# Performance work log

Measured on AMD Instinct MI355X. Metric: run time of the kernel, lower is better.

Reference implementation:

```python
import jax, jax.numpy as jnp
import numpy as np

N_NODES = 50000
N_EDGES = 800000
HIDDEN = 128
EPS = 1e-5


def _layernorm(x, g, b):
    m = jnp.mean(x, axis=-1, keepdims=True)
    v = jnp.var(x, axis=-1, keepdims=True)
    return (x - m) / jnp.sqrt(v + EPS) * g + b


def _batchnorm(x, g, b):
    # training-mode BatchNorm1d: stats over the node (batch) axis, biased var
    m = jnp.mean(x, axis=0, keepdims=True)
    v = jnp.var(x, axis=0, keepdims=True)
    return (x - m) / jnp.sqrt(v + EPS) * g + b


def _instnorm(x):
    # torch InstanceNorm1d on a 2D [N,C] input: unbatched (C,L) view ->
    # normalize each row over the feature axis, no affine params
    m = jnp.mean(x, axis=-1, keepdims=True)
    v = jnp.var(x, axis=-1, keepdims=True)
    return (x - m) / jnp.sqrt(v + EPS)


def _gcn_conv(x, W, b, row, col, norm, n):
    # PyG GCNConv: out[col] += norm * (x @ W)[row]; + bias
    xw = x @ W
    msgs = xw[row] * norm[:, None]          # [E+N, H]
    out = jax.ops.segment_sum(msgs, col, num_segments=n)
    return out + b


def setup_inputs() -> dict:
    key = jax.random.key(0)
    ks = jax.random.split(key, 12)
    H = HIDDEN
    x = jax.random.normal(ks[0], (N_NODES, 2), dtype=jnp.float32)
    edge_index = jax.random.randint(ks[1], (2, N_EDGES), 0, N_NODES, dtype=jnp.int64)

    def lin(k, fan_in, shape):
        bound = 1.0 / np.sqrt(fan_in)
        return jax.random.uniform(k, shape, jnp.float32, -bound, bound)

    inp = {
        "x": x,
        "edge_index": edge_index,
        "coord_W": lin(ks[2], 2, (2, H)),
        "coord_b": lin(ks[3], 2, (H,)),
        "ln_g": jnp.ones((H,), jnp.float32),
        "ln_b": jnp.zeros((H,), jnp.float32),
        "bn_g": jnp.ones((H,), jnp.float32),
        "bn_b": jnp.zeros((H,), jnp.float32),
        "W1": lin(ks[4], H, (H, H)),
        "b1": jnp.zeros((H,), jnp.float32),
        "W2": lin(ks[5], H, (H, H)),
        "b2": jnp.zeros((H,), jnp.float32),
        "W3": lin(ks[6], H, (H, H)),
        "b3": jnp.zeros((H,), jnp.float32),
        "fc1_W": lin(ks[7], H, (H, 32)),
        "fc1_b": lin(ks[8], H, (32,)),
        "fc2_W": lin(ks[9], 32, (32, 2)),
        "fc2_b": lin(ks[10], 32, (2,)),
    }
    return inp


def reference(x, edge_index, coord_W, coord_b, ln_g, ln_b, bn_g, bn_b,
              W1, b1, W2, b2, W3, b3, fc1_W, fc1_b, fc2_W, fc2_b):
    n = x.shape[0]
    loop = jnp.arange(n, dtype=edge_index.dtype)
    row = jnp.concatenate([edge_index[0], loop])
    col = jnp.concatenate([edge_index[1], loop])
    deg = jax.ops.segment_sum(jnp.ones_like(col, dtype=x.dtype), col, num_segments=n)
    dinv = 1.0 / jnp.sqrt(deg)              # deg >= 1 thanks to self-loops
    norm = dinv[row] * dinv[col]

    h = jax.nn.relu(x @ coord_W + coord_b)
    h = _layernorm(h, ln_g, ln_b)

    for W, b in ((W1, b1), (W2, b2), (W3, b3)):
        identity = h
        h = jax.nn.relu(_gcn_conv(h, W, b, row, col, norm, n))
        h = _batchnorm(h, bn_g, bn_b)
        h = _instnorm(h + identity)

    h = jax.nn.relu(h @ fc1_W + fc1_b)
    return jnp.tanh(h @ fc2_W + fc2_b)
```

## Files before the change

### kernel.cpp

```cpp
#include <hip/hip_runtime.h>
#include <hip/hip_bf16.h>
#include <hip/hip_fp16.h>
#include <stdint.h>

#define NN 50000
#define NE 800000
#define HD 128
#define EPSN 1e-5f
#define CAP 1152000

typedef __hip_bfloat16 bf16;
typedef __attribute__((ext_vector_type(8))) _Float16 half8;
typedef __attribute__((ext_vector_type(4))) float f32x4;

__device__ __forceinline__ float us2f(unsigned short u) { return __uint_as_float((uint32_t)u << 16); }
__device__ __forceinline__ ushort f2us(float f) {
    bf16 b = __float2bfloat16(f);
    return *reinterpret_cast<ushort*>(&b);
}
__device__ __forceinline__ ushort f2h(float f) {
    __half h = __float2half(f);
    return *reinterpret_cast<ushort*>(&h);
}
__device__ __forceinline__ float h2f(ushort u) {
    __half h = *reinterpret_cast<__half*>(&u);
    return __half2float(h);
}

__device__ __forceinline__ void cvt8(float4 v, float* o) {
    uint32_t a = __float_as_uint(v.x), b = __float_as_uint(v.y);
    uint32_t c = __float_as_uint(v.z), d = __float_as_uint(v.w);
    o[0] = h2f((ushort)(a & 0xffff)); o[1] = h2f((ushort)(a >> 16));
    o[2] = h2f((ushort)(b & 0xffff)); o[3] = h2f((ushort)(b >> 16));
    o[4] = h2f((ushort)(c & 0xffff)); o[5] = h2f((ushort)(c >> 16));
    o[6] = h2f((ushort)(d & 0xffff)); o[7] = h2f((ushort)(d >> 16));
}

#define O_X    0
#define O_CW   100000
#define O_CB   100256
#define O_LNG  100384
#define O_LNB  100512
#define O_BNG  100640
#define O_BNB  100768
#define O_W1   100896
#define O_B1   117280
#define O_W2   117408
#define O_B2   133792
#define O_W3   133920
#define O_B3   150304
#define O_F1W  150432
#define O_F1B  154528
#define O_F2W  154560
#define O_F2B  154624
#define O_TOT  154626

struct Ptrs { const void* p[17]; };

__device__ const int SEG_OFF[18] = {O_X, O_CW, O_CB, O_LNG, O_LNB, O_BNG, O_BNB,
                                    O_W1, O_B1, O_W2, O_B2, O_W3, O_B3,
                                    O_F1W, O_F1B, O_F2W, O_F2B, O_TOT};

__device__ __forceinline__ int eidx(const int* __restrict__ ei, int isL, int which, int e) {
    size_t base = (size_t)which * NE + e;
    return isL ? ei[2 * base] : ei[base];
}

__global__ void k_detect(const int* __restrict__ ei, const ushort* __restrict__ cw,
                         int* __restrict__ flags) {
    int t = threadIdx.x;
    int v = ei[2 * t + 1] | ei[1000000 + 2 * t + 1];
    int bad = 0;
    if (t < 128) {
        float val = us2f(cw[2 * t]);
        bad = !(fabsf(val) <= 1.0f);
    }
    for (int o = 32; o; o >>= 1) { v |= __shfl_xor(v, o); bad |= __shfl_xor(bad, o); }
    __shared__ int sv[4], sb[4];
    if ((t & 63) == 0) { sv[t >> 6] = v; sb[t >> 6] = bad; }
    __syncthreads();
    if (t == 0) {
        flags[0] = ((sv[0] | sv[1] | sv[2] | sv[3]) == 0) ? 1 : 0;
        flags[1] = ((sb[0] | sb[1] | sb[2] | sb[3]) == 0) ? 1 : 0;
    }
}

__global__ void k_conv(Ptrs ptrs, const int* __restrict__ flags, float* __restrict__ cp,
                       _Float16* __restrict__ wt, int* __restrict__ degR,
                       float* __restrict__ stats, int* __restrict__ cursor) {
    int i = blockIdx.x * 256 + threadIdx.x;
    int isBf = flags[1];
    if (i < O_TOT) {
        int s = 0;
        while (i >= SEG_OFF[s + 1]) s++;
        int local = i - SEG_OFF[s];
        const void* src = ptrs.p[s];
        cp[i] = isBf ? us2f(((const ushort*)src)[local]) : ((const float*)src)[local];
    }
    if (i < 3 * HD * HD) {
        int mat = i >> 14, idx = i & (HD * HD - 1);
        int k = idx >> 7, n = idx & 127;
        const void* src = ptrs.p[7 + 2 * mat];
        int local = k * HD + n;
        float v = isBf ? us2f(((const ushort*)src)[local]) : ((const float*)src)[local];
        wt[mat * HD * HD + n * HD + k] = (_Float16)v;
    }
    if (i < 8 * NN) degR[i] = (i < NN) ? 1 : 0;
    if (i < 12288) stats[i] = 0.f;
    if (i == 0) *cursor = 0;
}

__global__ void k_deg(const int* __restrict__ ei, const int* __restrict__ flags,
                      int* __restrict__ degR) {
    int e = blockIdx.x * 256 + threadIdx.x;
    if (e < NE) atomicAdd(&degR[(blockIdx.x & 7) * NN + eidx(ei, flags[0], 1, e)], 1);
}

__global__ void k_fill(const int* __restrict__ ei, const int* __restrict__ flags,
                       const float* __restrict__ dinv, int* __restrict__ curA8,
                       int2* __restrict__ srw) {
    int e = blockIdx.x * 256 + threadIdx.x;
    if (e >= NE) return;
    int isL = flags[0];
    int r = eidx(ei, isL, 0, e);
    int c = eidx(ei, isL, 1, e);
    int p = atomicAdd(&curA8[(blockIdx.x & 7) * NN + c], 1);
    srw[p] = make_int2(r << 4, __float_as_int(dinv[r]));
}


__global__ void k_embed(const float* __restrict__ cp, ushort* __restrict__ h,
                        const int* __restrict__ degR, float* __restrict__ dinv,
                        int* __restrict__ startA, int* __restrict__ curA8,
                        int* __restrict__ cursor, int2* __restrict__ srw,
                        int* __restrict__ degO) {
    int gi = blockIdx.x * 256 + threadIdx.x;
    if (gi < NN) {
        int c[8];
        int d = 0;
#pragma unroll
        for (int r = 0; r < 8; r++) { c[r] = degR[r * NN + gi]; d += c[r]; }
        c[0] -= 1;
        degO[gi] = d;
        dinv[gi] = rsqrtf((float)d);
        int cnt = d - 1;
        int cpad = (cnt + 7) & ~7;
        int s = atomicAdd(cursor, cpad);
        startA[gi] = s;
        int off = 0;
#pragma unroll
        for (int r = 0; r < 8; r++) { curA8[r * NN + gi] = s + off; off += c[r]; }
        for (int p = s + cnt; p < s + cpad; p++) srw[p] = make_int2(0, 0);
    }
    int node = gi >> 6;
    int lane = threadIdx.x & 63;
    if (node >= NN) return;
    const float* X = cp + O_X;
    const float* CW = cp + O_CW;
    const float* CB = cp + O_CB;
    const float* LG = cp + O_LNG;
    const float* LB = cp + O_LNB;
    float x0 = X[node * 2], x1 = X[node * 2 + 1];
    int f0 = lane, f1 = lane + 64;
    float v0 = fmaxf(0.f, x0 * CW[f0] + x1 * CW[HD + f0] + CB[f0]);
    float v1 = fmaxf(0.f, x0 * CW[f1] + x1 * CW[HD + f1] + CB[f1]);
    float s = v0 + v1, q = v0 * v0 + v1 * v1;
    for (int o = 32; o; o >>= 1) { s += __shfl_xor(s, o); q += __shfl_xor(q, o); }
    float m = s * (1.f / HD);
    float var = q * (1.f / HD) - m * m;
    float r = rsqrtf(var + EPSN);
    h[(size_t)node * HD + f0] = f2h((v0 - m) * r * LG[f0] + LB[f0]);
    h[(size_t)node * HD + f1] = f2h((v1 - m) * r * LG[f1] + LB[f1]);
}


__device__ __forceinline__ void mfma_tile(const _Float16* hl, const _Float16* __restrict__ wt,
                                          ushort* __restrict__ t0h, int nodeBase, int t) {
    int w = t >> 6, l = t & 63;
    int m16 = l & 15;
    int kg = l >> 4;
    int node0 = w * 16;
    half8 a[4];
#pragma unroll
    for (int kc = 0; kc < 4; kc++) {
        int nd = node0 + m16;
        int c16 = kc * 4 + kg;
        int chunk = nd * 16 + (c16 ^ (nd & 7));
        a[kc] = *(const half8*)(hl + chunk * 8);
    }
    f32x4 acc[8];
#pragma unroll
    for (int nt = 0; nt < 8; nt++) acc[nt] = (f32x4){0.f, 0.f, 0.f, 0.f};
#pragma unroll
    for (int nt = 0; nt < 8; nt++) {
        const half8* bp = (const half8*)(wt + (size_t)(nt * 16 + m16) * HD);
#pragma unroll
        for (int kc = 0; kc < 4; kc++) {
            acc[nt] = __builtin_amdgcn_mfma_f32_16x16x32_f16(a[kc], bp[kc * 4 + kg],
                                                             acc[nt], 0, 0, 0);
        }
    }
    int ndb = nodeBase + node0 + kg * 4;
#pragma unroll
    for (int rr = 0; rr < 4; rr++) {
        int nd = ndb + rr;
        if (nd < NN) {
#pragma unroll
            for (int nt = 0; nt < 8; nt++) {
                t0h[(size_t)nd * HD + nt * 16 + m16] = f2h(acc[nt][rr]);
            }
        }
    }
}


__global__ __launch_bounds__(256) void k_gemm(const ushort* __restrict__ h,
                                              const _Float16* __restrict__ wt,
                                              ushort* __restrict__ t0h) {
    __shared__ _Float16 hl[64 * HD];
    int t = threadIdx.x;
    int nodeBase = blockIdx.x * 64;
    const uint4* h4 = (const uint4*)h;
#pragma unroll
    for (int r = 0; r < 4; r++) {
        int cid = r * 256 + t;
        int node = cid >> 4;
        int c16 = cid & 15;
        int n = nodeBase + node;
        uint4 v = make_uint4(0u, 0u, 0u, 0u);
        if (n < NN) v = h4[(size_t)n * 16 + c16];
        int chunk = node * 16 + (c16 ^ (node & 7));
        *(uint4*)(hl + chunk * 8) = v;
    }
    __syncthreads();
    mfma_tile(hl, wt, t0h, nodeBase, t);
}


__global__ __launch_bounds__(256) void k_gemm_fused(const float* __restrict__ agg,
                                                    const float* __restrict__ stats,
                                                    const float* __restrict__ bias,
                                                    const float* __restrict__ bng,
                                                    const float* __restrict__ bnb,
                                                    ushort* __restrict__ h,
                                                    const _Float16* __restrict__ wt,
                                                    ushort* __restrict__ t0h) {
    __shared__ _Float16 hl[64 * HD];
    __shared__ float scL[HD], shL[HD], bL[HD];
    int t = threadIdx.x;
    if (t < 128) {
        const float invN = 1.f / NN;
        float sv = 0.f, qv = 0.f;
#pragma unroll
        for (int r = 0; r < 16; r++) { sv += stats[r * 256 + t]; qv += stats[r * 256 + 128 + t]; }
        float m = sv * invN;
        float v = qv * invN - m * m;
        float sc = bng[t] * rsqrtf(v + EPSN);
        scL[t] = sc;
        shL[t] = bnb[t] - m * sc;
        bL[t] = bias[t];
    }
    __syncthreads();
    int nodeBase = blockIdx.x * 64;
    const float4* a4 = (const float4*)agg;
    const ushort4* h4r = (const ushort4*)h;
    ushort4* h4w = (ushort4*)h;
#pragma unroll
    for (int r = 0; r < 8; r++) {
        int idx = r * 256 + t;
        int node = idx >> 5;
        int c4 = idx & 31;
        int n = nodeBase + node;
        float4 u = make_float4(0.f, 0.f, 0.f, 0.f);
        if (n < NN) {
            float4 av = a4[(size_t)n * 32 + c4];
            ushort4 hv = h4r[(size_t)n * 32 + c4];
            int f = c4 * 4;
            float y0 = fmaxf(0.f, av.x + bL[f]);
            float y1 = fmaxf(0.f, av.y + bL[f + 1]);
            float y2 = fmaxf(0.f, av.z + bL[f + 2]);
            float y3 = fmaxf(0.f, av.w + bL[f + 3]);
            u.x = y0 * scL[f]     + shL[f]     + h2f(hv.x);
            u.y = y1 * scL[f + 1] + shL[f + 1] + h2f(hv.y);
            u.z = y2 * scL[f + 2] + shL[f + 2] + h2f(hv.z);
            u.w = y3 * scL[f + 3] + shL[f + 3] + h2f(hv.w);
        }
        float s = u.x + u.y + u.z + u.w;
        float q = u.x * u.x + u.y * u.y + u.z * u.z + u.w * u.w;
        for (int o = 16; o; o >>= 1) { s += __shfl_xor(s, o); q += __shfl_xor(q, o); }
        float m = s * (1.f / HD);
        float var = q * (1.f / HD) - m * m;
        float rr = rsqrtf(var + EPSN);
        u.x = (u.x - m) * rr; u.y = (u.y - m) * rr;
        u.z = (u.z - m) * rr; u.w = (u.w - m) * rr;
        ushort4 pk;
        pk.x = f2h(u.x); pk.y = f2h(u.y); pk.z = f2h(u.z); pk.w = f2h(u.w);
        if (n < NN) h4w[(size_t)n * 32 + c4] = pk;
        int chunk = node * 16 + ((c4 >> 1) ^ (node & 7));
        *(ushort4*)((char*)hl + chunk * 16 + (c4 & 1) * 8) = pk;
    }
    __syncthreads();
    mfma_tile(hl, wt, t0h, nodeBase, t);
}


__global__ __launch_bounds__(256) void k_agg(const ushort* __restrict__ t0h,
                                             const int2* __restrict__ srw,
                                             const int* __restrict__ startA,
                                             const int* __restrict__ deg,
                                             const float* __restrict__ dinv,
                                             const float* __restrict__ bias,
                                             float* __restrict__ agg,
                                             float* __restrict__ stats) {
    int t = threadIdx.x;
    int w = t >> 6;
    int l = t & 63;
    int g = l >> 4;
    int k = l & 15;
    int l32 = l & 31;
    const float4* t04 = (const float4*)t0h;
    float4* agg4 = (float4*)agg;
    float bs[8];
    {
        const float4* b4 = (const float4*)bias;
        float4 u0 = b4[2 * k], u1 = b4[2 * k + 1];
        bs[0] = u0.x; bs[1] = u0.y; bs[2] = u0.z; bs[3] = u0.w;
        bs[4] = u1.x; bs[5] = u1.y; bs[6] = u1.z; bs[7] = u1.w;
    }
    float rs1[8], rs2[8];
#pragma unroll
    for (int m = 0; m < 8; m++) { rs1[m] = 0.f; rs2[m] = 0.f; }
    int stride = gridDim.x * 4;
    int i = blockIdx.x * 4 + w;
    int s = 0, nb = 0;
    float di = 0.f;
    if (i < NN) {
        s = startA[i];
        nb = (deg[i] - 1 + 7) & ~7;
        di = dinv[i];
    }
    while (i < NN) {
        float4 sv = t04[(size_t)i * 16 + k];
        int2 e = make_int2(0, 0);
        if (l32 < nb) e = srw[s + l32];
        int ex = e.x, ey = e.y;
        int nb4 = nb >> 2;
        float4 gg[8];
#define GATH(b) { int rv = __shfl(ex, 4 * (b) + g); \
                  gg[b] = t04[(size_t)(uint32_t)rv + k]; }
        if (nb4 > 0) { GATH(0) GATH(1) }
        if (nb4 > 2) { GATH(2) GATH(3) }
        if (nb4 > 4) { GATH(4) GATH(5) }
        if (nb4 > 6) { GATH(6) GATH(7) }
#undef GATH
        int inext = i + stride;
        int sN = 0, nbN = 0;
        float diN = 0.f;
        if (inext < NN) {
            sN = startA[inext];
            nbN = (deg[inext] - 1 + 7) & ~7;
            diN = dinv[inext];
        }
        float acc[8], c8[8];
        cvt8(sv, c8);
        float ws = (g == 0) ? di : 0.f;
#pragma unroll
        for (int m = 0; m < 8; m++) acc[m] = ws * c8[m];
#define ACCB(b) { float wv = __int_as_float(__shfl(ey, 4 * (b) + g)); \
                  float d8[8]; cvt8(gg[b], d8); \
                  _Pragma("unroll") \
                  for (int m = 0; m < 8; m++) acc[m] += wv * d8[m]; }
        if (nb4 > 0) { ACCB(0) ACCB(1) }
        if (nb4 > 2) { ACCB(2) ACCB(3) }
        if (nb4 > 4) { ACCB(4) ACCB(5) }
        if (nb4 > 6) { ACCB(6) ACCB(7) }
#undef ACCB
        for (int j = 32; j < nb; j += 32) {
            int2 e2 = make_int2(0, 0);
            if (j + l32 < nb) e2 = srw[s + j + l32];
            int ex2 = e2.x, ey2 = e2.y;
            int rem4 = (nb - j) >> 2;
            if (rem4 > 8) rem4 = 8;
            for (int b = 0; b < rem4; b += 2) {
                int r0 = __shfl(ex2, 4 * b + g);
                int r1 = __shfl(ex2, 4 * b + 4 + g);
                float4 g0 = t04[(size_t)(uint32_t)r0 + k];
                float4 g1 = t04[(size_t)(uint32_t)r1 + k];
                float w0 = __int_as_float(__shfl(ey2, 4 * b + g));
                float w1 = __int_as_float(__shfl(ey2, 4 * b + 4 + g));
                float d0[8], d1[8];
                cvt8(g0, d0); cvt8(g1, d1);
#pragma unroll
                for (int m = 0; m < 8; m++) acc[m] += w0 * d0[m] + w1 * d1[m];
            }
        }
#pragma unroll
        for (int m = 0; m < 8; m++) {
            acc[m] += __shfl_xor(acc[m], 16);
            acc[m] += __shfl_xor(acc[m], 32);
            acc[m] *= di;
        }
        if (g == 0) {
            agg4[(size_t)i * 32 + 2 * k]     = make_float4(acc[0], acc[1], acc[2], acc[3]);
            agg4[(size_t)i * 32 + 2 * k + 1] = make_float4(acc[4], acc[5], acc[6], acc[7]);
        }
#pragma unroll
        for (int m = 0; m < 8; m++) {
            float y = fmaxf(0.f, acc[m] + bs[m]);
            rs1[m] += y;
            rs2[m] += y * y;
        }
        i = inext; s = sN; nb = nbN; di = diN;
    }
    __shared__ float s1[4][HD], s2[4][HD];
    if (l < 16) {
#pragma unroll
        for (int m = 0; m < 8; m++) {
            s1[w][k * 8 + m] = rs1[m];
            s2[w][k * 8 + m] = rs2[m];
        }
    }
    __syncthreads();
    float* st = stats + (blockIdx.x & 15) * 256;
    if (t < 128) {
        atomicAdd(&st[t], s1[0][t] + s1[1][t] + s1[2][t] + s1[3][t]);
    } else {
        int f = t - 128;
        atomicAdd(&st[128 + f], s2[0][f] + s2[1][f] + s2[2][f] + s2[3][f]);
    }
}


__global__ __launch_bounds__(256) void k_tail(const float* __restrict__ agg,
                                              const float* __restrict__ stats,
                                              const ushort* __restrict__ h,
                                              const float* __restrict__ cp,
                                              const int* __restrict__ flags,
                                              void* __restrict__ outv) {
    __shared__ float W1l[HD * 32];
    __shared__ float ub[4][HD];
    __shared__ float scT[HD], shT[HD], bT[HD];
    __shared__ float B1s[32], W2s[64], B2s[2];
    int t = threadIdx.x;
    const float4* f1w4 = (const float4*)(cp + O_F1W);
    float4* w14 = (float4*)W1l;
#pragma unroll
    for (int r = 0; r < 4; r++) w14[r * 256 + t] = f1w4[r * 256 + t];
    if (t < 32) B1s[t] = cp[O_F1B + t];
    if (t < 64) W2s[t] = cp[O_F2W + t];
    if (t < 2) B2s[t] = cp[O_F2B + t];
    if (t < 128) {
        const float invN = 1.f / NN;
        float sv = 0.f, qv = 0.f;
#pragma unroll
        for (int r = 0; r < 16; r++) { sv += stats[r * 256 + t]; qv += stats[r * 256 + 128 + t]; }
        float m = sv * invN;
        float v = qv * invN - m * m;
        float sc = cp[O_BNG + t] * rsqrtf(v + EPSN);
        scT[t] = sc;
        shT[t] = cp[O_BNB + t] - m * sc;
        bT[t] = cp[O_B3 + t];
    }
    __syncthreads();
    int isBf = flags[1];
    int w = t >> 6, l = t & 63;
    int f = l & 31, half = l >> 5;
    for (int base = blockIdx.x * 4; base < NN; base += gridDim.x * 4) {
        int node = base + w;
        if (node >= NN) continue;
        size_t o = (size_t)node * HD;
        float a0 = agg[o + l], a1 = agg[o + l + 64];
        float h0 = h2f(h[o + l]), h1 = h2f(h[o + l + 64]);
        float y0 = fmaxf(0.f, a0 + bT[l]);
        float y1 = fmaxf(0.f, a1 + bT[l + 64]);
        float u0 = y0 * scT[l]      + shT[l]      + h0;
        float u1 = y1 * scT[l + 64] + shT[l + 64] + h1;
        float s = u0 + u1, q = u0 * u0 + u1 * u1;
        for (int oo = 32; oo; oo >>= 1) { s += __shfl_xor(s, oo); q += __shfl_xor(q, oo); }
        float m = s * (1.f / HD);
        float var = q * (1.f / HD) - m * m;
        float r = rsqrtf(var + EPSN);
        u0 = (u0 - m) * r; u1 = (u1 - m) * r;
        ub[w][l] = u0; ub[w][l + 64] = u1;
        float acc = (half == 0) ? B1s[f] : 0.f;
        const float* up = ub[w] + half * 64;
        const float* wp = W1l + half * 64 * 32 + f;
#pragma unroll 16
        for (int kk = 0; kk < 64; kk++) acc += up[kk] * wp[kk * 32];
        acc += __shfl_xor(acc, 32);
        float av = fmaxf(0.f, acc);
        float p0 = av * W2s[f * 2], p1 = av * W2s[f * 2 + 1];
        for (int oo = 16; oo; oo >>= 1) { p0 += __shfl_xor(p0, oo); p1 += __shfl_xor(p1, oo); }
        if (l == 0) {
            p0 = tanhf(p0 + B2s[0]); p1 = tanhf(p1 + B2s[1]);
            if (isBf) {
                ((uint32_t*)outv)[node] = (uint32_t)f2us(p0) | ((uint32_t)f2us(p1) << 16);
            } else {
                float2 ov; ov.x = p0; ov.y = p1;
                ((float2*)outv)[node] = ov;
            }
        }
    }
}


extern "C" void kernel_launch(void* const* d_in, const int* in_sizes, int n_in,
                              void* d_out, int out_size, void* d_ws, size_t ws_size,
                              hipStream_t stream) {
    const int* ei = (const int*)d_in[1];

    Ptrs ptrs;
    ptrs.p[0] = d_in[0];
    for (int s = 1; s < 17; s++) ptrs.p[s] = d_in[s + 1];

    char* wsp = (char*)d_ws;
    size_t off = 0;
    auto alloc = [&](size_t bytes) {
        void* p = wsp + off;
        off += (bytes + 255) & ~(size_t)255;
        return p;
    };
    float* cp     = (float*)alloc((size_t)O_TOT * 4);
    ushort* h     = (ushort*)alloc((size_t)NN * HD * 2);
    ushort* t0h   = (ushort*)alloc((size_t)NN * HD * 2);
    float* agg    = (float*)alloc((size_t)NN * HD * 4);
    int* degR     = (int*)alloc((size_t)8 * NN * 4);
    int* degO     = (int*)alloc((size_t)NN * 4);
    float* dinv   = (float*)alloc((size_t)NN * 4);
    int2* srw     = (int2*)alloc((size_t)CAP * 8);
    int* startA   = (int*)alloc((size_t)NN * 4);
    int* curA8    = (int*)alloc((size_t)8 * NN * 4);
    float* stats  = (float*)alloc(3 * 4096 * 4);
    int* cursor   = (int*)alloc(256);
    int* flags    = (int*)alloc(256);
    _Float16* wt  = (_Float16*)alloc((size_t)3 * HD * HD * 2);

    const int BN_EDGE = (NE + 255) / 256;
    const int BN_CONV = (8 * NN + 255) / 256;
    const int BN_GEMM = (NN + 63) / 64;

    const float* B[3] = {cp + O_B1, cp + O_B2, cp + O_B3};

    k_detect<<<1, 256, 0, stream>>>(ei, (const ushort*)d_in[2], flags);
    k_conv<<<BN_CONV, 256, 0, stream>>>(ptrs, flags, cp, wt, degR, stats, cursor);
    k_deg<<<BN_EDGE, 256, 0, stream>>>(ei, flags, degR);
    k_embed<<<NN / 4, 256, 0, stream>>>(cp, h, degR, dinv, startA, curA8, cursor, srw, degO);
    k_fill<<<BN_EDGE, 256, 0, stream>>>(ei, flags, dinv, curA8, srw);

    k_gemm<<<BN_GEMM, 256, 0, stream>>>(h, wt, t0h);
    k_agg<<<2048, 256, 0, stream>>>(t0h, srw, startA, degO, dinv, B[0], agg, stats);
    for (int l = 1; l < 3; l++) {
        k_gemm_fused<<<BN_GEMM, 256, 0, stream>>>(agg, stats + 4096 * (l - 1),
                                                  B[l - 1], cp + O_BNG, cp + O_BNB,
                                                  h, wt + (size_t)l * HD * HD, t0h);
        k_agg<<<2048, 256, 0, stream>>>(t0h, srw, startA, degO, dinv, B[l],
                                        agg, stats + 4096 * l);
    }
    k_tail<<<2048, 256, 0, stream>>>(agg, stats + 8192, h, cp, flags, d_out);
}
```

Before: 445.0 us.

## Fold source dinv into GEMM epilogue and shrink edge records to int

Multiplies each GEMM output row by its own dinv so the aggregation kernel only sums gathered rows, with the destination dinv applied afterward as before. Edge records drop from int2 (index plus weight) to a single int, which halves CSR traffic and removes the weight shuffles and multiplies in the gather loop. Padding slots now point to an extra zeroed row at index NN instead of carrying weight zero. This needs one more row in t0h, and pre-scaling before the fp16 store slightly changes rounding.

Result: faster. 414.5 us (-6.9%).

```diff
diff --git a/kernel.cpp b/kernel.cpp
--- a/kernel.cpp
+++ b/kernel.cpp
@@ -87,7 +87,8 @@
 
 __global__ void k_conv(Ptrs ptrs, const int* __restrict__ flags, float* __restrict__ cp,
                        _Float16* __restrict__ wt, int* __restrict__ degR,
-                       float* __restrict__ stats, int* __restrict__ cursor) {
+                       float* __restrict__ stats, int* __restrict__ cursor,
+                       ushort* __restrict__ t0h) {
     int i = blockIdx.x * 256 + threadIdx.x;
     int isBf = flags[1];
     if (i < O_TOT) {
@@ -107,6 +108,7 @@
     }
     if (i < 8 * NN) degR[i] = (i < NN) ? 1 : 0;
     if (i < 12288) stats[i] = 0.f;
+    if (i < HD) t0h[(size_t)NN * HD + i] = 0;
     if (i == 0) *cursor = 0;
 }
 
@@ -117,22 +119,21 @@
 }
 
 __global__ void k_fill(const int* __restrict__ ei, const int* __restrict__ flags,
-                       const float* __restrict__ dinv, int* __restrict__ curA8,
-                       int2* __restrict__ srw) {
+                       int* __restrict__ curA8, int* __restrict__ srw) {
     int e = blockIdx.x * 256 + threadIdx.x;
     if (e >= NE) return;
     int isL = flags[0];
     int r = eidx(ei, isL, 0, e);
     int c = eidx(ei, isL, 1, e);
     int p = atomicAdd(&curA8[(blockIdx.x & 7) * NN + c], 1);
-    srw[p] = make_int2(r << 4, __float_as_int(dinv[r]));
+    srw[p] = r << 4;
 }
 
 
 __global__ void k_embed(const float* __restrict__ cp, ushort* __restrict__ h,
                         const int* __restrict__ degR, float* __restrict__ dinv,
                         int* __restrict__ startA, int* __restrict__ curA8,
-                        int* __restrict__ cursor, int2* __restrict__ srw,
+                        int* __restrict__ cursor, int* __restrict__ srw,
                         int* __restrict__ degO) {
     int gi = blockIdx.x * 256 + threadIdx.x;
     if (gi < NN) {
@@ -150,7 +151,7 @@
         int off = 0;
 #pragma unroll
         for (int r = 0; r < 8; r++) { curA8[r * NN + gi] = s + off; off += c[r]; }
-        for (int p = s + cnt; p < s + cpad; p++) srw[p] = make_int2(0, 0);
+        for (int p = s + cnt; p < s + cpad; p++) srw[p] = NN << 4;
     }
     int node = gi >> 6;
     int lane = threadIdx.x & 63;
@@ -175,6 +176,7 @@
 
 
 __device__ __forceinline__ void mfma_tile(const _Float16* hl, const _Float16* __restrict__ wt,
+                                          const float* __restrict__ dinv,
                                           ushort* __restrict__ t0h, int nodeBase, int t) {
     int w = t >> 6, l = t & 63;
     int m16 = l & 15;
@@ -205,9 +207,10 @@
     for (int rr = 0; rr < 4; rr++) {
         int nd = ndb + rr;
         if (nd < NN) {
+            float dv = dinv[nd];
 #pragma unroll
             for (int nt = 0; nt < 8; nt++) {
-                t0h[(size_t)nd * HD + nt * 16 + m16] = f2h(acc[nt][rr]);
+                t0h[(size_t)nd * HD + nt * 16 + m16] = f2h(acc[nt][rr] * dv);
             }
         }
     }
@@ -216,6 +219,7 @@
 
 __global__ __launch_bounds__(256) void k_gemm(const ushort* __restrict__ h,
                                               const _Float16* __restrict__ wt,
+                                              const float* __restrict__ dinv,
                                               ushort* __restrict__ t0h) {
     __shared__ _Float16 hl[64 * HD];
     int t = threadIdx.x;
@@ -233,7 +237,7 @@
         *(uint4*)(hl + chunk * 8) = v;
     }
     __syncthreads();
-    mfma_tile(hl, wt, t0h, nodeBase, t);
+    mfma_tile(hl, wt, dinv, t0h, nodeBase, t);
 }
 
 
@@ -244,6 +248,7 @@
                                                     const float* __restrict__ bnb,
                                                     ushort* __restrict__ h,
                                                     const _Float16* __restrict__ wt,
+                                                    const float* __restrict__ dinv,
                                                     ushort* __restrict__ t0h) {
     __shared__ _Float16 hl[64 * HD];
     __shared__ float scL[HD], shL[HD], bL[HD];
@@ -300,12 +305,12 @@
         *(ushort4*)((char*)hl + chunk * 16 + (c4 & 1) * 8) = pk;
     }
     __syncthreads();
-    mfma_tile(hl, wt, t0h, nodeBase, t);
+    mfma_tile(hl, wt, dinv, t0h, nodeBase, t);
 }
 
 
 __global__ __launch_bounds__(256) void k_agg(const ushort* __restrict__ t0h,
-                                             const int2* __restrict__ srw,
+                                             const int* __restrict__ srw,
                                              const int* __restrict__ startA,
                                              const int* __restrict__ deg,
                                              const float* __restrict__ dinv,
@@ -341,9 +346,8 @@
     }
     while (i < NN) {
         float4 sv = t04[(size_t)i * 16 + k];
-        int2 e = make_int2(0, 0);
-        if (l32 < nb) e = srw[s + l32];
-        int ex = e.x, ey = e.y;
+        int ex = 0;
+        if (l32 < nb) ex = srw[s + l32];
         int nb4 = nb >> 2;
         float4 gg[8];
 #define GATH(b) { int rv = __shfl(ex, 4 * (b) + g); \
@@ -363,22 +367,20 @@
         }
         float acc[8], c8[8];
         cvt8(sv, c8);
-        float ws = (g == 0) ? di : 0.f;
+        float ws = (g == 0) ? 1.f : 0.f;
 #pragma unroll
         for (int m = 0; m < 8; m++) acc[m] = ws * c8[m];
-#define ACCB(b) { float wv = __int_as_float(__shfl(ey, 4 * (b) + g)); \
-                  float d8[8]; cvt8(gg[b], d8); \
+#define ACCB(b) { float d8[8]; cvt8(gg[b], d8); \
                   _Pragma("unroll") \
-                  for (int m = 0; m < 8; m++) acc[m] += wv * d8[m]; }
+                  for (int m = 0; m < 8; m++) acc[m] += d8[m]; }
         if (nb4 > 0) { ACCB(0) ACCB(1) }
         if (nb4 > 2) { ACCB(2) ACCB(3) }
         if (nb4 > 4) { ACCB(4) ACCB(5) }
         if (nb4 > 6) { ACCB(6) ACCB(7) }
 #undef ACCB
         for (int j = 32; j < nb; j += 32) {
-            int2 e2 = make_int2(0, 0);
-            if (j + l32 < nb) e2 = srw[s + j + l32];
-            int ex2 = e2.x, ey2 = e2.y;
+            int ex2 = 0;
+            if (j + l32 < nb) ex2 = srw[s + j + l32];
             int rem4 = (nb - j) >> 2;
             if (rem4 > 8) rem4 = 8;
             for (int b = 0; b < rem4; b += 2) {
@@ -386,12 +388,10 @@
                 int r1 = __shfl(ex2, 4 * b + 4 + g);
                 float4 g0 = t04[(size_t)(uint32_t)r0 + k];
                 float4 g1 = t04[(size_t)(uint32_t)r1 + k];
-                float w0 = __int_as_float(__shfl(ey2, 4 * b + g));
-                float w1 = __int_as_float(__shfl(ey2, 4 * b + 4 + g));
                 float d0[8], d1[8];
                 cvt8(g0, d0); cvt8(g1, d1);
 #pragma unroll
-                for (int m = 0; m < 8; m++) acc[m] += w0 * d0[m] + w1 * d1[m];
+                for (int m = 0; m < 8; m++) acc[m] += d0[m] + d1[m];
             }
         }
 #pragma unroll
@@ -522,12 +522,12 @@
     };
     float* cp     = (float*)alloc((size_t)O_TOT * 4);
     ushort* h     = (ushort*)alloc((size_t)NN * HD * 2);
-    ushort* t0h   = (ushort*)alloc((size_t)NN * HD * 2);
+    ushort* t0h   = (ushort*)alloc((size_t)(NN + 1) * HD * 2);
     float* agg    = (float*)alloc((size_t)NN * HD * 4);
     int* degR     = (int*)alloc((size_t)8 * NN * 4);
     int* degO     = (int*)alloc((size_t)NN * 4);
     float* dinv   = (float*)alloc((size_t)NN * 4);
-    int2* srw     = (int2*)alloc((size_t)CAP * 8);
+    int* srw      = (int*)alloc((size_t)CAP * 4);
     int* startA   = (int*)alloc((size_t)NN * 4);
     int* curA8    = (int*)alloc((size_t)8 * NN * 4);
     float* stats  = (float*)alloc(3 * 4096 * 4);
@@ -542,17 +542,17 @@
     const float* B[3] = {cp + O_B1, cp + O_B2, cp + O_B3};
 
     k_detect<<<1, 256, 0, stream>>>(ei, (const ushort*)d_in[2], flags);
-    k_conv<<<BN_CONV, 256, 0, stream>>>(ptrs, flags, cp, wt, degR, stats, cursor);
+    k_conv<<<BN_CONV, 256, 0, stream>>>(ptrs, flags, cp, wt, degR, stats, cursor, t0h);
     k_deg<<<BN_EDGE, 256, 0, stream>>>(ei, flags, degR);
     k_embed<<<NN / 4, 256, 0, stream>>>(cp, h, degR, dinv, startA, curA8, cursor, srw, degO);
-    k_fill<<<BN_EDGE, 256, 0, stream>>>(ei, flags, dinv, curA8, srw);
-
-    k_gemm<<<BN_GEMM, 256, 0, stream>>>(h, wt, t0h);
+    k_fill<<<BN_EDGE, 256, 0, stream>>>(ei, flags, curA8, srw);
+
+    k_gemm<<<BN_GEMM, 256, 0, stream>>>(h, wt, dinv, t0h);
     k_agg<<<2048, 256, 0, stream>>>(t0h, srw, startA, degO, dinv, B[0], agg, stats);
     for (int l = 1; l < 3; l++) {
         k_gemm_fused<<<BN_GEMM, 256, 0, stream>>>(agg, stats + 4096 * (l - 1),
                                                   B[l - 1], cp + O_BNG, cp + O_BNB,
-                                                  h, wt + (size_t)l * HD * HD, t0h);
+                                                  h, wt + (size_t)l * HD * HD, dinv, t0h);
         k_agg<<<2048, 256, 0, stream>>>(t0h, srw, startA, degO, dinv, B[l],
                                         agg, stats + 4096 * l);
     }
```
